# Kernel optimization log

Measured on AMD Instinct MI355X. Metric: run time of the kernel, lower is better.

## Reference

```python
import jax, jax.numpy as jnp
import numpy as np

N_NODES = 100000
IN_DIM = 256
HIDDEN = 512
N_INC = 1000000   # incidence (gather/scatter) list length
N_SEG = 100000    # number of hyperedges / segments


def setup_inputs() -> dict:
    key = jax.random.key(0)
    ks = jax.random.split(key, 6)
    x = jax.random.normal(ks[0], (N_NODES, IN_DIM), dtype=jnp.float32)
    target_nodes = jax.random.randint(ks[1], (N_INC,), 0, N_NODES, dtype=jnp.int32)
    target_ids = jnp.sort(jax.random.randint(ks[2], (N_INC,), 0, N_SEG, dtype=jnp.int32))
    # Linear params (PyTorch stores [out,in]; we keep [in,out] and matmul directly)
    W1 = jax.random.normal(ks[3], (IN_DIM, HIDDEN), dtype=jnp.float32) * (1.0 / np.sqrt(IN_DIM))
    b1 = jnp.zeros((HIDDEN,), dtype=jnp.float32)
    W2 = jax.random.normal(ks[4], (HIDDEN, 1), dtype=jnp.float32) * (1.0 / np.sqrt(HIDDEN))
    b2 = jnp.zeros((1,), dtype=jnp.float32)
    return {"x": x, "target_nodes": target_nodes, "target_ids": target_ids,
            "num_segments": N_SEG, "W1": W1, "b1": b1, "W2": W2, "b2": b2}


def reference(x, target_nodes, target_ids, num_segments, W1, b1, W2, b2):
    # gather node features, scatter-sum into segments (hyperedges)
    gathered = x[target_nodes, :]                                   # [N_INC, IN_DIM]
    Z = jax.ops.segment_sum(gathered, target_ids,
                            num_segments=num_segments)              # [N_SEG, IN_DIM]
    Z = jnp.maximum(Z @ W1 + b1, 0.0)                               # linear + relu
    # dropout is identity in eval mode
    Z = Z @ W2 + b2                                                 # [N_SEG, 1]
    return jax.nn.sigmoid(Z)[:, 0]                                  # squeeze(-1)
```

## Files before the change

kernel.cpp:

```cpp
#include <hip/hip_runtime.h>
#include <hip/hip_bf16.h>
#include <math.h>

#define N_NODES   100000
#define IN_DIM    256
#define HIDDEN    512
#define N_INC     1000000
#define N_SEG     100000

typedef __attribute__((ext_vector_type(8))) short bf16x8;
typedef __attribute__((ext_vector_type(4))) float f32x4;

__device__ __forceinline__ unsigned short f2bf(float f) {
  unsigned int u = __builtin_bit_cast(unsigned int, f);
  u += 0x7FFFu + ((u >> 16) & 1u);
  return (unsigned short)(u >> 16);
}
__device__ __forceinline__ float bflo(unsigned int u) {
  return __builtin_bit_cast(float, u << 16);
}
__device__ __forceinline__ float bfhi(unsigned int u) {
  return __builtin_bit_cast(float, u & 0xFFFF0000u);
}
__device__ __forceinline__ unsigned pack2(float a, float b) {
  return (unsigned)f2bf(a) | ((unsigned)f2bf(b) << 16);
}

#define XBF_BLOCKS    25000
#define STARTS_BLOCKS 391
#define W1T_BLOCKS    128

__global__ void k_prep(const float* __restrict__ x, unsigned short* __restrict__ xb,
                       const int* __restrict__ ids, int* __restrict__ starts,
                       const float* __restrict__ W1, unsigned short* __restrict__ W1t) {
  const int b = blockIdx.x;
  const int tid = threadIdx.x;
  if (b < XBF_BLOCKS) {
    size_t idx = (size_t)b * 256 + tid;
    float4 v = *(const float4*)(x + idx * 4);
    uint2 p;
    p.x = pack2(v.x, v.y);
    p.y = pack2(v.z, v.w);
    *(uint2*)(xb + idx * 4) = p;
  } else if (b < XBF_BLOCKS + STARTS_BLOCKS) {
    int s = (b - XBF_BLOCKS) * 256 + tid;
    if (s > N_SEG) return;
    int lo = 0, hi = N_INC;
    while (lo < hi) {
      int mid = (lo + hi) >> 1;
      if (ids[mid] < s) lo = mid + 1; else hi = mid;
    }
    starts[s] = lo;
  } else {
    int idx = (b - XBF_BLOCKS - STARTS_BLOCKS) * 256 + tid;
    int k  = idx >> 7;
    int c4 = idx & 127;
    float4 v = *(const float4*)(W1 + (size_t)k * HIDDEN + c4 * 4);
    W1t[(c4 * 4 + 0) * IN_DIM + k] = f2bf(v.x);
    W1t[(c4 * 4 + 1) * IN_DIM + k] = f2bf(v.y);
    W1t[(c4 * 4 + 2) * IN_DIM + k] = f2bf(v.z);
    W1t[(c4 * 4 + 3) * IN_DIM + k] = f2bf(v.w);
  }
}

#define ACC8(v)                                                        \
  acc0 += bflo((v).x); acc1 += bfhi((v).x);                            \
  acc2 += bflo((v).y); acc3 += bfhi((v).y);                            \
  acc4 += bflo((v).z); acc5 += bfhi((v).z);                            \
  acc6 += bflo((v).w); acc7 += bfhi((v).w);

__global__ void k_segsum(const unsigned short* __restrict__ xb, const int* __restrict__ nodes,
                         const int* __restrict__ starts, unsigned short* __restrict__ Zb) {
  int wave = threadIdx.x >> 6;
  int lane = threadIdx.x & 63;
  int s = blockIdx.x * 4 + wave;
  if (s >= N_SEG) return;
  const int beg = starts[s];
  const int end = starts[s + 1];
  const int half = lane >> 5;
  const int sl   = lane & 31;
  const unsigned short* base = xb + sl * 8;
  float acc0 = 0.f, acc1 = 0.f, acc2 = 0.f, acc3 = 0.f;
  float acc4 = 0.f, acc5 = 0.f, acc6 = 0.f, acc7 = 0.f;
  int j = beg + half;
  for (; j + 6 < end; j += 8) {
    int n0 = nodes[j], n1 = nodes[j + 2], n2 = nodes[j + 4], n3 = nodes[j + 6];
    uint4 v0 = *(const uint4*)(base + (size_t)n0 * IN_DIM);
    uint4 v1 = *(const uint4*)(base + (size_t)n1 * IN_DIM);
    uint4 v2 = *(const uint4*)(base + (size_t)n2 * IN_DIM);
    uint4 v3 = *(const uint4*)(base + (size_t)n3 * IN_DIM);
    ACC8(v0); ACC8(v1); ACC8(v2); ACC8(v3);
  }
  for (; j < end; j += 2) {
    int n0 = nodes[j];
    uint4 v0 = *(const uint4*)(base + (size_t)n0 * IN_DIM);
    ACC8(v0);
  }
  acc0 += __shfl_xor(acc0, 32, 64);
  acc1 += __shfl_xor(acc1, 32, 64);
  acc2 += __shfl_xor(acc2, 32, 64);
  acc3 += __shfl_xor(acc3, 32, 64);
  acc4 += __shfl_xor(acc4, 32, 64);
  acc5 += __shfl_xor(acc5, 32, 64);
  acc6 += __shfl_xor(acc6, 32, 64);
  acc7 += __shfl_xor(acc7, 32, 64);
  if (half == 0) {
    uint4 p;
    p.x = pack2(acc0, acc1);
    p.y = pack2(acc2, acc3);
    p.z = pack2(acc4, acc5);
    p.w = pack2(acc6, acc7);
    *(uint4*)(Zb + (size_t)s * IN_DIM + sl * 8) = p;
  }
}

__global__ __launch_bounds__(256, 2) void k_mlp(
    const unsigned short* __restrict__ Zb, const unsigned short* __restrict__ W1t,
    const float* __restrict__ b1, const float* __restrict__ W2,
    const float* __restrict__ b2, float* __restrict__ out) {
  __shared__ __align__(16) unsigned short Bf[8][4][64][8];
  const int tid  = threadIdx.x;
  const int wave = tid >> 6;
  const int lane = tid & 63;
  const int m0   = blockIdx.x * 256 + wave * 64;

  uint4 a[4][8];
  const int arow = m0 + (lane & 15);
  const int ak   = (lane >> 4) * 8;
  #pragma unroll
  for (int kc = 0; kc < 8; ++kc) {
    #pragma unroll
    for (int rf = 0; rf < 4; ++rf) {
      int row = arow + rf * 16;
      if (row < N_SEG)
        a[rf][kc] = *(const uint4*)(Zb + (size_t)row * IN_DIM + kc * 32 + ak);
      else
        a[rf][kc] = make_uint4(0u, 0u, 0u, 0u);
    }
  }

  float logit[4][4];
  #pragma unroll
  for (int rf = 0; rf < 4; ++rf)
    #pragma unroll
    for (int e = 0; e < 4; ++e) logit[rf][e] = 0.f;

  for (int nt = 0; nt < 8; ++nt) {
    const int c0 = nt * 64;
    #pragma unroll
    for (int it = 0; it < 8; ++it) {
      int idx = it * 256 + tid;
      int kc  = idx >> 8;
      int rem = idx & 255;
      int cf  = rem >> 6;
      int l2  = rem & 63;
      int col = c0 + cf * 16 + (l2 & 15);
      int kk  = kc * 32 + (l2 >> 4) * 8;
      *(uint4*)&Bf[kc][cf][l2][0] = *(const uint4*)(W1t + col * IN_DIM + kk);
    }
    __syncthreads();

    f32x4 acc[4][4];
    #pragma unroll
    for (int rf = 0; rf < 4; ++rf)
      #pragma unroll
      for (int cf = 0; cf < 4; ++cf) acc[rf][cf] = (f32x4){0.f, 0.f, 0.f, 0.f};

    #pragma unroll
    for (int kc = 0; kc < 8; ++kc) {
      #pragma unroll
      for (int cf = 0; cf < 4; ++cf) {
        bf16x8 bv = *(const bf16x8*)&Bf[kc][cf][lane][0];
        #pragma unroll
        for (int rf = 0; rf < 4; ++rf) {
          bf16x8 av = __builtin_bit_cast(bf16x8, a[rf][kc]);
          acc[rf][cf] = __builtin_amdgcn_mfma_f32_16x16x32_bf16(av, bv, acc[rf][cf], 0, 0, 0);
        }
      }
    }
    __syncthreads();

    #pragma unroll
    for (int cf = 0; cf < 4; ++cf) {
      int c = c0 + cf * 16 + (lane & 15);
      float bb = b1[c];
      float w2 = W2[c];
      #pragma unroll
      for (int rf = 0; rf < 4; ++rf)
        #pragma unroll
        for (int e = 0; e < 4; ++e) {
          float h = acc[rf][cf][e] + bb;
          h = h > 0.f ? h : 0.f;
          logit[rf][e] = fmaf(h, w2, logit[rf][e]);
        }
    }
  }
  #pragma unroll
  for (int rf = 0; rf < 4; ++rf)
    #pragma unroll
    for (int e = 0; e < 4; ++e) {
      float v = logit[rf][e];
      v += __shfl_xor(v, 1, 64);
      v += __shfl_xor(v, 2, 64);
      v += __shfl_xor(v, 4, 64);
      v += __shfl_xor(v, 8, 64);
      logit[rf][e] = v;
    }
  if ((lane & 15) == 0) {
    float bb2 = b2[0];
    #pragma unroll
    for (int rf = 0; rf < 4; ++rf)
      #pragma unroll
      for (int e = 0; e < 4; ++e) {
        int row = m0 + rf * 16 + (lane >> 4) * 4 + e;
        if (row < N_SEG)
          out[row] = 1.f / (1.f + expf(-(logit[rf][e] + bb2)));
      }
  }
}

extern "C" void kernel_launch(void* const* d_in, const int* in_sizes, int n_in,
                              void* d_out, int out_size, void* d_ws, size_t ws_size,
                              hipStream_t stream) {
  const float* x   = (const float*)d_in[0];
  const int* nodes = (const int*)d_in[1];
  const int* ids   = (const int*)d_in[2];
  const float* W1  = (const float*)d_in[4];
  const float* b1  = (const float*)d_in[5];
  const float* W2  = (const float*)d_in[6];
  const float* b2  = (const float*)d_in[7];
  float* out       = (float*)d_out;

  char* ws = (char*)d_ws;
  int* starts = (int*)ws;
  size_t off = (((size_t)(N_SEG + 1) * sizeof(int)) + 1023) & ~(size_t)1023;
  unsigned short* Zb = (unsigned short*)(ws + off);
  off += (size_t)N_NODES * IN_DIM * sizeof(unsigned short);
  off = (off + 1023) & ~(size_t)1023;
  unsigned short* W1t = (unsigned short*)(ws + off);
  off += (size_t)HIDDEN * IN_DIM * sizeof(unsigned short);
  off = (off + 1023) & ~(size_t)1023;
  unsigned short* xb = (unsigned short*)(ws + off);

  k_prep<<<XBF_BLOCKS + STARTS_BLOCKS + W1T_BLOCKS, 256, 0, stream>>>(
      x, xb, ids, starts, W1, W1t);
  k_segsum<<<(N_SEG + 3) / 4, 256, 0, stream>>>(xb, nodes, starts, Zb);
  k_mlp<<<(N_SEG + 255) / 256, 256, 0, stream>>>(Zb, W1t, b1, W2, b2, out);
}
```

Measured before the change: 158.7 us.

## Chunk bf16 node features by column and node-half for cache-local gather

The bf16 copy of x is now stored as 16 slabs, one per 32-column chunk and node half, so each slab is about 3.2 MB. The segment-sum kernel assigns blocks to one column chunk and loops over the two node halves, gathering only nodes in the current half. The aim is to keep the working set of random gathers resident in L2/MALL instead of thrashing across the full 51 MB table. The cost is that node indices are read 16 times (8 chunks × 2 halves), the inner loop branches on the half test, and each access is only 64 bytes, which may underuse memory transactions.

```diff
diff --git a/kernel.cpp b/kernel.cpp
--- a/kernel.cpp
+++ b/kernel.cpp
@@ -7,6 +7,7 @@
 #define HIDDEN    512
 #define N_INC     1000000
 #define N_SEG     100000
+#define NHALF     50000
 
 typedef __attribute__((ext_vector_type(8))) short bf16x8;
 typedef __attribute__((ext_vector_type(4))) float f32x4;
@@ -30,18 +31,24 @@
 #define STARTS_BLOCKS 391
 #define W1T_BLOCKS    128
 
-__global__ void k_prep(const float* __restrict__ x, unsigned short* __restrict__ xb,
+__global__ void k_prep(const float* __restrict__ x, unsigned short* __restrict__ xbc,
                        const int* __restrict__ ids, int* __restrict__ starts,
                        const float* __restrict__ W1, unsigned short* __restrict__ W1t) {
   const int b = blockIdx.x;
   const int tid = threadIdx.x;
   if (b < XBF_BLOCKS) {
     size_t idx = (size_t)b * 256 + tid;
-    float4 v = *(const float4*)(x + idx * 4);
+    int n = (int)(idx >> 6);
+    int q = (int)(idx & 63);
+    float4 v = *(const float4*)(x + (size_t)n * IN_DIM + q * 4);
+    int c  = q >> 3;
+    int h  = n >= NHALF;
+    int np = n - h * NHALF;
+    size_t dst = ((size_t)(c * 2 + h) * NHALF + np) * 32 + (q & 7) * 4;
     uint2 p;
     p.x = pack2(v.x, v.y);
     p.y = pack2(v.z, v.w);
-    *(uint2*)(xb + idx * 4) = p;
+    *(uint2*)(xbc + dst) = p;
   } else if (b < XBF_BLOCKS + STARTS_BLOCKS) {
     int s = (b - XBF_BLOCKS) * 256 + tid;
     if (s > N_SEG) return;
@@ -64,53 +71,52 @@
 }
 
 #define ACC8(v)                                                        \
-  acc0 += bflo((v).x); acc1 += bfhi((v).x);                            \
-  acc2 += bflo((v).y); acc3 += bfhi((v).y);                            \
-  acc4 += bflo((v).z); acc5 += bfhi((v).z);                            \
-  acc6 += bflo((v).w); acc7 += bfhi((v).w);
-
-__global__ void k_segsum(const unsigned short* __restrict__ xb, const int* __restrict__ nodes,
+  a0 += bflo((v).x); a1 += bfhi((v).x);                                \
+  a2 += bflo((v).y); a3 += bfhi((v).y);                                \
+  a4 += bflo((v).z); a5 += bfhi((v).z);                                \
+  a6 += bflo((v).w); a7 += bfhi((v).w);
+
+__global__ void k_segsum(const unsigned short* __restrict__ xbc, const int* __restrict__ nodes,
                          const int* __restrict__ starts, unsigned short* __restrict__ Zb) {
-  int wave = threadIdx.x >> 6;
-  int lane = threadIdx.x & 63;
-  int s = blockIdx.x * 4 + wave;
-  if (s >= N_SEG) return;
-  const int beg = starts[s];
-  const int end = starts[s + 1];
-  const int half = lane >> 5;
-  const int sl   = lane & 31;
-  const unsigned short* base = xb + sl * 8;
-  float acc0 = 0.f, acc1 = 0.f, acc2 = 0.f, acc3 = 0.f;
-  float acc4 = 0.f, acc5 = 0.f, acc6 = 0.f, acc7 = 0.f;
-  int j = beg + half;
-  for (; j + 6 < end; j += 8) {
-    int n0 = nodes[j], n1 = nodes[j + 2], n2 = nodes[j + 4], n3 = nodes[j + 6];
-    uint4 v0 = *(const uint4*)(base + (size_t)n0 * IN_DIM);
-    uint4 v1 = *(const uint4*)(base + (size_t)n1 * IN_DIM);
-    uint4 v2 = *(const uint4*)(base + (size_t)n2 * IN_DIM);
-    uint4 v3 = *(const uint4*)(base + (size_t)n3 * IN_DIM);
-    ACC8(v0); ACC8(v1); ACC8(v2); ACC8(v3);
-  }
-  for (; j < end; j += 2) {
-    int n0 = nodes[j];
-    uint4 v0 = *(const uint4*)(base + (size_t)n0 * IN_DIM);
-    ACC8(v0);
-  }
-  acc0 += __shfl_xor(acc0, 32, 64);
-  acc1 += __shfl_xor(acc1, 32, 64);
-  acc2 += __shfl_xor(acc2, 32, 64);
-  acc3 += __shfl_xor(acc3, 32, 64);
-  acc4 += __shfl_xor(acc4, 32, 64);
-  acc5 += __shfl_xor(acc5, 32, 64);
-  acc6 += __shfl_xor(acc6, 32, 64);
-  acc7 += __shfl_xor(acc7, 32, 64);
-  if (half == 0) {
+  const int lane = threadIdx.x & 63;
+  const int wv   = threadIdx.x >> 6;
+  const int c    = blockIdx.x & 7;
+  const int grp  = blockIdx.x >> 3;
+  const int seg_slot = lane >> 4;
+  const int inc_lane = (lane >> 2) & 3;
+  const int dim_lane = lane & 3;
+  const int s = (grp * 4 + wv) * 4 + seg_slot;
+  int beg = 0, end = 0;
+  if (s < N_SEG) { beg = starts[s]; end = starts[s + 1]; }
+  float a0 = 0.f, a1 = 0.f, a2 = 0.f, a3 = 0.f;
+  float a4 = 0.f, a5 = 0.f, a6 = 0.f, a7 = 0.f;
+  #pragma unroll
+  for (int h = 0; h < 2; ++h) {
+    const int lo = h * NHALF;
+    const unsigned short* base = xbc + ((size_t)(c * 2 + h) * NHALF) * 32 + dim_lane * 8;
+    for (int j = beg + inc_lane; j < end; j += 4) {
+      int n = nodes[j] - lo;
+      if ((unsigned)n < (unsigned)NHALF) {
+        uint4 v = *(const uint4*)(base + (size_t)n * 32);
+        ACC8(v);
+      }
+    }
+  }
+  a0 += __shfl_xor(a0, 4, 64);  a0 += __shfl_xor(a0, 8, 64);
+  a1 += __shfl_xor(a1, 4, 64);  a1 += __shfl_xor(a1, 8, 64);
+  a2 += __shfl_xor(a2, 4, 64);  a2 += __shfl_xor(a2, 8, 64);
+  a3 += __shfl_xor(a3, 4, 64);  a3 += __shfl_xor(a3, 8, 64);
+  a4 += __shfl_xor(a4, 4, 64);  a4 += __shfl_xor(a4, 8, 64);
+  a5 += __shfl_xor(a5, 4, 64);  a5 += __shfl_xor(a5, 8, 64);
+  a6 += __shfl_xor(a6, 4, 64);  a6 += __shfl_xor(a6, 8, 64);
+  a7 += __shfl_xor(a7, 4, 64);  a7 += __shfl_xor(a7, 8, 64);
+  if (inc_lane == 0 && s < N_SEG) {
     uint4 p;
-    p.x = pack2(acc0, acc1);
-    p.y = pack2(acc2, acc3);
-    p.z = pack2(acc4, acc5);
-    p.w = pack2(acc6, acc7);
-    *(uint4*)(Zb + (size_t)s * IN_DIM + sl * 8) = p;
+    p.x = pack2(a0, a1);
+    p.y = pack2(a2, a3);
+    p.z = pack2(a4, a5);
+    p.w = pack2(a6, a7);
+    *(uint4*)(Zb + (size_t)s * IN_DIM + c * 32 + dim_lane * 8) = p;
   }
 }
 
@@ -182,9 +188,9 @@
 
     #pragma unroll
     for (int cf = 0; cf < 4; ++cf) {
-      int c = c0 + cf * 16 + (lane & 15);
-      float bb = b1[c];
-      float w2 = W2[c];
+      int cc = c0 + cf * 16 + (lane & 15);
+      float bb = b1[cc];
+      float w2 = W2[cc];
       #pragma unroll
       for (int rf = 0; rf < 4; ++rf)
         #pragma unroll
@@ -240,10 +246,11 @@
   unsigned short* W1t = (unsigned short*)(ws + off);
   off += (size_t)HIDDEN * IN_DIM * sizeof(unsigned short);
   off = (off + 1023) & ~(size_t)1023;
-  unsigned short* xb = (unsigned short*)(ws + off);
+  unsigned short* xbc = (unsigned short*)(ws + off);
 
   k_prep<<<XBF_BLOCKS + STARTS_BLOCKS + W1T_BLOCKS, 256, 0, stream>>>(
-      x, xb, ids, starts, W1, W1t);
-  k_segsum<<<(N_SEG + 3) / 4, 256, 0, stream>>>(xb, nodes, starts, Zb);
+      x, xbc, ids, starts, W1, W1t);
+  int ngroups = (N_SEG + 15) / 16;
+  k_segsum<<<ngroups * 8, 256, 0, stream>>>(xbc, nodes, starts, Zb);
   k_mlp<<<(N_SEG + 255) / 256, 256, 0, stream>>>(Zb, W1t, b1, W2, b2, out);
 }
```

After: 254.9 us. 60.6% more time.
